# Kernel tuning notes

Measured on AMD Instinct MI355X. Metric: run time of the kernel, lower is better.

## Reference

```python
import jax, jax.numpy as jnp
import numpy as np

BN_EPS = 1e-5

def setup_inputs() -> dict:
    key = jax.random.key(0)
    ks = jax.random.split(key, 6)
    B, C, N = 8, 256, 4096
    da = C // 4
    return {
        "x": jax.random.normal(ks[0], (B, C, N), dtype=jnp.float32),
        "Wq": jax.random.normal(ks[1], (da, C), dtype=jnp.float32) * (C ** -0.5),
        "Wk": jax.random.normal(ks[2], (da, C), dtype=jnp.float32) * (C ** -0.5),
        "Wv": jax.random.normal(ks[3], (C, C), dtype=jnp.float32) * (C ** -0.5),
        "Wp": jax.random.normal(ks[4], (C, C), dtype=jnp.float32) * (C ** -0.5),
        "bn_gamma": jnp.ones((C,), dtype=jnp.float32),
        "bn_beta": jnp.zeros((C,), dtype=jnp.float32),
        "bn_mean": jnp.zeros((C,), dtype=jnp.float32),
        "bn_var": jnp.ones((C,), dtype=jnp.float32),
    }

def reference(x, Wq, Wk, Wv, Wp, bn_gamma, bn_beta, bn_mean, bn_var):
    # x: [B, C, N]; 1x1 Conv1d == channel matmul
    q = jnp.einsum('bcn,dc->bnd', x, Wq)          # [B, N, da]
    k = jnp.einsum('bcn,dc->bdn', x, Wk)          # [B, da, N]
    v = jnp.einsum('bcn,dc->bnd', x, Wv)          # [B, N, C]
    energy = jnp.einsum('bnd,bdm->bnm', q, k)     # [B, N, N]
    # offset-attention double normalization: softmax over dim=1 (rows), then L1 over dim=-1
    attn = jax.nn.softmax(energy, axis=1)
    attn = attn / (1e-9 + attn.sum(axis=-1, keepdims=True))
    fsa = jnp.einsum('bnm,bmc->bcn', attn, v)     # [B, C, N]
    y = x - fsa
    h = jnp.einsum('bcn,dc->bdn', y, Wp)          # 1x1 conv of LBR
    # BatchNorm1d (inference-mode with running stats)
    inv = bn_gamma / jnp.sqrt(bn_var + BN_EPS)
    h = h * inv[None, :, None] + (bn_beta - bn_mean * inv)[None, :, None]
    return jax.nn.relu(h) + x
```

## Files before the change

### kernel.cpp

```cpp
#include <hip/hip_runtime.h>
#include <math.h>

#define BD 8
#define CD 256
#define ND 4096
#define DA 64
#define CT 272

typedef __attribute__((ext_vector_type(8))) short short8v;
typedef __attribute__((ext_vector_type(4))) float float4v;

static __device__ __forceinline__ float4v mfma16(short8v a, short8v b, float4v c) {
  return __builtin_amdgcn_mfma_f32_16x16x32_bf16(a, b, c, 0, 0, 0);
}
static __device__ __forceinline__ unsigned short f2bf(float f) {
  union { float f; unsigned int u; } v; v.f = f;
  return (unsigned short)((v.u + 0x7fffu + ((v.u >> 16) & 1u)) >> 16);
}
static __device__ __forceinline__ float bf2f(unsigned short h) {
  union { unsigned int u; float f; } v; v.u = (unsigned int)h << 16;
  return v.f;
}
static __device__ __forceinline__ int sw(int row, int c8) {
  return row * 64 + (((c8) ^ (row & 7)) << 3);
}
typedef const __attribute__((address_space(1))) unsigned int g_u32;
typedef __attribute__((address_space(3))) unsigned int l_u32;
static __device__ __forceinline__ void gld16(const void* g, void* l) {
  __builtin_amdgcn_global_load_lds((g_u32*)g, (l_u32*)l, 16, 0, 0);
}

__global__ __launch_bounds__(256) void k_prep(const float* __restrict__ x,
                                              unsigned short* __restrict__ xTh,
                                              unsigned short* __restrict__ xTl) {
  const int n0 = blockIdx.x * 64, c0 = blockIdx.y * 64, b = blockIdx.z;
  __shared__ float Xs[64][68];
  const int tid = threadIdx.x;
  const int r0 = tid >> 4, col4 = (tid & 15) * 4;
#pragma unroll
  for (int j = 0; j < 4; ++j) {
    int r = r0 + j * 16;
    *(float4*)&Xs[r][col4] =
        *(const float4*)&x[((size_t)(b * CD + c0 + r)) * ND + n0 + col4];
  }
  __syncthreads();
  const int n = tid >> 2, cg = (tid & 3) * 16;
  unsigned short h[16], l[16];
#pragma unroll
  for (int j = 0; j < 16; ++j) {
    float v = Xs[cg + j][n];
    h[j] = f2bf(v);
    l[j] = f2bf(v - bf2f(h[j]));
  }
  size_t o = ((size_t)b * ND + n0 + n) * CD + c0 + cg;
#pragma unroll
  for (int j = 0; j < 4; ++j) {
    *(ushort4*)&xTh[o + j * 4] = *(ushort4*)&h[j * 4];
    *(ushort4*)&xTl[o + j * 4] = *(ushort4*)&l[j * 4];
  }
}

__global__ void k_prepW(const float* __restrict__ Wq, const float* __restrict__ Wk,
                        const float* __restrict__ Wv, const float* __restrict__ Wp,
                        unsigned short* Wqh, unsigned short* Wql,
                        unsigned short* Wkh, unsigned short* Wkl,
                        unsigned short* Wvh, unsigned short* Wvl,
                        unsigned short* Wph, unsigned short* Wpl) {
  int i = blockIdx.x * 256 + threadIdx.x;
  int row = i >> 6, c4 = (i & 63) * 4;
  const float* src; unsigned short *dh, *dl; int r;
  if (row < 64)       { src = Wq; dh = Wqh; dl = Wql; r = row; }
  else if (row < 128) { src = Wk; dh = Wkh; dl = Wkl; r = row - 64; }
  else if (row < 384) { src = Wv; dh = Wvh; dl = Wvl; r = row - 128; }
  else                { src = Wp; dh = Wph; dl = Wpl; r = row - 384; }
  float4 f = *(const float4*)&src[(size_t)r * 256 + c4];
  ushort4 hh, ll;
  hh.x = f2bf(f.x); hh.y = f2bf(f.y); hh.z = f2bf(f.z); hh.w = f2bf(f.w);
  ll.x = f2bf(f.x - bf2f(hh.x)); ll.y = f2bf(f.y - bf2f(hh.y));
  ll.z = f2bf(f.z - bf2f(hh.z)); ll.w = f2bf(f.w - bf2f(hh.w));
  *(ushort4*)&dh[(size_t)r * 256 + c4] = hh;
  *(ushort4*)&dl[(size_t)r * 256 + c4] = ll;
}

__global__ __launch_bounds__(256, 4) void k_proj64(
    const unsigned short* __restrict__ xTh, const unsigned short* __restrict__ xTl,
    const unsigned short* __restrict__ Wh, const unsigned short* __restrict__ Wl,
    unsigned short* __restrict__ oh, unsigned short* __restrict__ ol) {
  const int n0 = blockIdx.x * 128, b = blockIdx.y;
  const int tid = threadIdx.x, w = tid >> 6, lane = tid & 63, lq = lane & 15,
            quad = lane >> 4;
  const int nh = w & 1, dh = w >> 1;
  float4v O[2][4];
#pragma unroll
  for (int dt = 0; dt < 2; ++dt)
#pragma unroll
    for (int nt = 0; nt < 4; ++nt) O[dt][nt] = (float4v){0.f, 0.f, 0.f, 0.f};
#pragma unroll 2
  for (int ks = 0; ks < 8; ++ks) {
    short8v awh[2], awl[2], bxh[4], bxl[4];
#pragma unroll
    for (int dt = 0; dt < 2; ++dt) {
      size_t a = (size_t)(dh * 32 + dt * 16 + lq) * CD + ks * 32 + quad * 8;
      awh[dt] = *(const short8v*)(Wh + a);
      awl[dt] = *(const short8v*)(Wl + a);
    }
#pragma unroll
    for (int nt = 0; nt < 4; ++nt) {
      size_t a = ((size_t)b * ND + n0 + nh * 64 + nt * 16 + lq) * CD + ks * 32 + quad * 8;
      bxh[nt] = *(const short8v*)(xTh + a);
      bxl[nt] = *(const short8v*)(xTl + a);
    }
#pragma unroll
    for (int dt = 0; dt < 2; ++dt)
#pragma unroll
      for (int nt = 0; nt < 4; ++nt) {
        O[dt][nt] = mfma16(awh[dt], bxh[nt], O[dt][nt]);
        O[dt][nt] = mfma16(awl[dt], bxh[nt], O[dt][nt]);
        O[dt][nt] = mfma16(awh[dt], bxl[nt], O[dt][nt]);
      }
  }
#pragma unroll
  for (int dt = 0; dt < 2; ++dt)
#pragma unroll
    for (int nt = 0; nt < 4; ++nt) {
      int d0v = dh * 32 + dt * 16 + quad * 4;
      int n = n0 + nh * 64 + nt * 16 + lq;
      ushort4 hh, ll;
      float v0 = O[dt][nt][0], v1 = O[dt][nt][1], v2 = O[dt][nt][2], v3 = O[dt][nt][3];
      hh.x = f2bf(v0); hh.y = f2bf(v1); hh.z = f2bf(v2); hh.w = f2bf(v3);
      ll.x = f2bf(v0 - bf2f(hh.x)); ll.y = f2bf(v1 - bf2f(hh.y));
      ll.z = f2bf(v2 - bf2f(hh.z)); ll.w = f2bf(v3 - bf2f(hh.w));
      size_t o = ((size_t)b * ND + n) * DA + d0v;
      *(ushort4*)&oh[o] = hh;
      *(ushort4*)&ol[o] = ll;
    }
}

__global__ __launch_bounds__(256, 4) void k_projvT(
    const unsigned short* __restrict__ xTh, const unsigned short* __restrict__ xTl,
    const unsigned short* __restrict__ Wvh, const unsigned short* __restrict__ Wvl,
    unsigned short* __restrict__ vT) {
  const int m0 = blockIdx.x * 128, cob = blockIdx.y * 64, b = blockIdx.z;
  const int tid = threadIdx.x, w = tid >> 6, lane = tid & 63, lq = lane & 15,
            quad = lane >> 4;
  const int mh = w & 1, ch2 = w >> 1;
  float4v O[2][4];
#pragma unroll
  for (int ct = 0; ct < 2; ++ct)
#pragma unroll
    for (int mt = 0; mt < 4; ++mt) O[ct][mt] = (float4v){0.f, 0.f, 0.f, 0.f};
#pragma unroll 2
  for (int ks = 0; ks < 8; ++ks) {
    short8v awh[2], awl[2], bxh[4], bxl[4];
#pragma unroll
    for (int ct = 0; ct < 2; ++ct) {
      size_t a = (size_t)(cob + ch2 * 32 + ct * 16 + lq) * CD + ks * 32 + quad * 8;
      awh[ct] = *(const short8v*)(Wvh + a);
      awl[ct] = *(const short8v*)(Wvl + a);
    }
#pragma unroll
    for (int mt = 0; mt < 4; ++mt) {
      size_t a = ((size_t)b * ND + m0 + mh * 64 + mt * 16 + lq) * CD + ks * 32 + quad * 8;
      bxh[mt] = *(const short8v*)(xTh + a);
      bxl[mt] = *(const short8v*)(xTl + a);
    }
#pragma unroll
    for (int ct = 0; ct < 2; ++ct)
#pragma unroll
      for (int mt = 0; mt < 4; ++mt) {
        O[ct][mt] = mfma16(awh[ct], bxh[mt], O[ct][mt]);
        O[ct][mt] = mfma16(awl[ct], bxh[mt], O[ct][mt]);
        O[ct][mt] = mfma16(awh[ct], bxl[mt], O[ct][mt]);
      }
  }
#pragma unroll
  for (int ct = 0; ct < 2; ++ct)
#pragma unroll
    for (int mt = 0; mt < 4; ++mt) {
      int m = m0 + mh * 64 + mt * 16 + lq;
#pragma unroll
      for (int r = 0; r < 4; ++r) {
        int co = cob + ch2 * 32 + ct * 16 + quad * 4 + r;
        vT[((size_t)b * CT + co) * ND + m] = f2bf(O[ct][mt][r]);
      }
    }
}

__global__ void k_fill(unsigned short* __restrict__ vT) {
  int i = blockIdx.x * 256 + threadIdx.x;
  int b = i >> 14, r = (i >> 10) & 15, n4 = i & 1023;
  unsigned short val = (r == 0) ? (unsigned short)0x3F80 : (unsigned short)0;
  ushort4 v; v.x = val; v.y = val; v.z = val; v.w = val;
  *(ushort4*)&vT[((size_t)b * CT + 256 + r) * ND + n4 * 4] = v;
}

__global__ __launch_bounds__(512, 4) void k_colsum(
    const unsigned short* __restrict__ qh, const unsigned short* __restrict__ ql,
    const unsigned short* __restrict__ kh, const unsigned short* __restrict__ kl,
    float* __restrict__ Dp) {
  const int bid = blockIdx.x, b = bid & 7, half = (bid >> 3) & 1,
            m0 = (bid >> 4) * 128;
  const int nbase = half * 2048;
  const int tid = threadIdx.x, w = tid >> 6, lane = tid & 63, lq = lane & 15,
            quad = lane >> 4;
  const int mq = w & 3, nh = w >> 2;
  __shared__ __align__(16) unsigned short qbuf[2][128 * 64];
  __shared__ float Cb[128];
  short8v bkh[2][2], bkl[2][2];
#pragma unroll
  for (int sub = 0; sub < 2; ++sub)
#pragma unroll
    for (int k = 0; k < 2; ++k) {
      size_t a = ((size_t)b * ND + m0 + mq * 32 + sub * 16 + lq) * DA + k * 32 + quad * 8;
      bkh[sub][k] = *(const short8v*)(kh + a);
      bkl[sub][k] = *(const short8v*)(kl + a);
    }
  uint4 sreg[2];
  const int srow = tid >> 3, sc8 = tid & 7;
  auto load_stage = [&](int nb) {
    sreg[0] = *(const uint4*)(qh + ((size_t)b * ND + nb + srow) * DA + sc8 * 8);
    sreg[1] = *(const uint4*)(ql + ((size_t)b * ND + nb + srow) * DA + sc8 * 8);
  };
  auto write_stage = [&](int buf) {
    *(uint4*)&qbuf[buf][sw(srow, sc8)] = sreg[0];
    *(uint4*)&qbuf[buf][sw(64 + srow, sc8)] = sreg[1];
  };
  load_stage(nbase); write_stage(0); load_stage(nbase + 64);
  __syncthreads();
  float cs0 = 0.f, cs1 = 0.f;
  for (int i = 0; i < 32; ++i) {
    const int cur = i & 1;
#pragma unroll
    for (int s = 0; s < 2; ++s) {
      short8v ah[2], al[2];
#pragma unroll
      for (int k = 0; k < 2; ++k) {
        ah[k] = *(const short8v*)&qbuf[cur][sw(nh * 32 + s * 16 + lq, k * 4 + quad)];
        al[k] = *(const short8v*)&qbuf[cur][sw(64 + nh * 32 + s * 16 + lq, k * 4 + quad)];
      }
#pragma unroll
      for (int sub = 0; sub < 2; ++sub) {
        float4v acc = {0.f, 0.f, 0.f, 0.f};
#pragma unroll
        for (int k = 0; k < 2; ++k) {
          acc = mfma16(ah[k], bkh[sub][k], acc);
          acc = mfma16(al[k], bkh[sub][k], acc);
          acc = mfma16(ah[k], bkl[sub][k], acc);
        }
        float e0 = __expf(acc[0]) + __expf(acc[1]) + __expf(acc[2]) + __expf(acc[3]);
        if (sub == 0) cs0 += e0; else cs1 += e0;
      }
    }
    if (i < 31) { write_stage(1 - cur); if (i < 30) load_stage(nbase + (i + 2) * 64); }
    __syncthreads();
  }
  cs0 += __shfl_down(cs0, 16); cs0 += __shfl_down(cs0, 32);
  cs1 += __shfl_down(cs1, 16); cs1 += __shfl_down(cs1, 32);
  if (nh == 0 && lane < 16) {
    Cb[mq * 32 + lane] = cs0;
    Cb[mq * 32 + 16 + lane] = cs1;
  }
  __syncthreads();
  if (nh == 1 && lane < 16) {
    float t0 = Cb[mq * 32 + lane] + cs0;
    float t1 = Cb[mq * 32 + 16 + lane] + cs1;
    size_t o = (size_t)half * (BD * ND) + (size_t)b * ND + m0 + mq * 32 + lane;
    Dp[o] = t0;
    Dp[o + 16] = t1;
  }
}

__global__ void k_rcp(const float* __restrict__ Dp, float* __restrict__ Drec) {
  int i = blockIdx.x * 256 + threadIdx.x;
  float4 a = *(const float4*)&Dp[(size_t)i * 4];
  float4 c = *(const float4*)&Dp[(size_t)(BD * ND) + (size_t)i * 4];
  float4 r;
  r.x = 1.f / (a.x + c.x); r.y = 1.f / (a.y + c.y);
  r.z = 1.f / (a.z + c.z); r.w = 1.f / (a.w + c.w);
  *(float4*)&Drec[(size_t)i * 4] = r;
}

__global__ __launch_bounds__(512, 2) void k_attn(
    const unsigned short* __restrict__ qh, const unsigned short* __restrict__ ql,
    const unsigned short* __restrict__ khp, const unsigned short* __restrict__ klp,
    const unsigned short* __restrict__ vT, const float* __restrict__ Drec,
    unsigned short* xhy, const unsigned short* __restrict__ xTl) {
  const int bid = blockIdx.x, b = bid & 7, n0 = (bid >> 3) * 128;
  const int tid = threadIdx.x, w = tid >> 6, lane = tid & 63, lq = lane & 15,
            quad = lane >> 4;
  const int nq = w & 3, ch = w >> 2;
  __shared__ __align__(16) unsigned short vbuf[3][CT * 64];
  __shared__ __align__(16) unsigned short Pb[2][128 * 64];
  __shared__ float DrecS[ND];
  __shared__ float Sb[128];

  short8v aq[2][2][2];
#pragma unroll
  for (int s = 0; s < 2; ++s)
#pragma unroll
    for (int k = 0; k < 2; ++k) {
      size_t a = ((size_t)b * ND + n0 + nq * 32 + s * 16 + lq) * DA + k * 32 + quad * 8;
      aq[s][k][0] = *(const short8v*)(qh + a);
      aq[s][k][1] = *(const short8v*)(ql + a);
    }
  float4v O[2][9];
#pragma unroll
  for (int s = 0; s < 2; ++s)
#pragma unroll
    for (int t = 0; t < 9; ++t) O[s][t] = (float4v){0.f, 0.f, 0.f, 0.f};

  auto stageV = [&](int mt, int vn) {
    unsigned short* base = &vbuf[vn][0];
#pragma unroll
    for (int j = 0; j < 4; ++j) {
      int cidx = tid + j * 512;
      int row = cidx >> 3, ckpos = cidx & 7;
      const unsigned short* src =
          vT + ((size_t)b * CT + row) * ND + mt * 64 + ((ckpos ^ (row & 7)) << 3);
      gld16(src, base + (size_t)(w * 64 + j * 512) * 8);
    }
    if (tid < 128) {
      int cidx = 2048 + tid;
      int row = cidx >> 3, ckpos = cidx & 7;
      const unsigned short* src =
          vT + ((size_t)b * CT + row) * ND + mt * 64 + ((ckpos ^ (row & 7)) << 3);
      gld16(src, base + (size_t)(2048 + w * 64) * 8);
    }
  };
  short8v kc[8], kn[8];
  auto kload = [&](short8v* dst, int mt) {
#pragma unroll
    for (int sub = 0; sub < 2; ++sub)
#pragma unroll
      for (int k = 0; k < 2; ++k) {
        size_t a = ((size_t)b * ND + mt * 64 + ch * 32 + sub * 16 + lq) * DA +
                   k * 32 + quad * 8;
        dst[sub * 4 + k * 2 + 0] = *(const short8v*)(khp + a);
        dst[sub * 4 + k * 2 + 1] = *(const short8v*)(klp + a);
      }
  };

  stageV(0, 0);
  kload(kc, 0);
  for (int idx = tid; idx < ND / 4; idx += 512)
    *(float4*)&DrecS[idx * 4] = *(const float4*)&Drec[(size_t)b * ND + idx * 4];
  __syncthreads();

  int vn = 0;
#pragma unroll 1
  for (int i = 0; i < 64; ++i) {
    int vnext = vn + 1; if (vnext == 3) vnext = 0;
    if (i < 63) { stageV(i + 1, vnext); kload(kn, i + 1); }
    unsigned short* Pcur = &Pb[i & 1][0];
#pragma unroll
    for (int sub = 0; sub < 2; ++sub) {
      const int m_loc = ch * 32 + sub * 16 + lq;
      const float dr = DrecS[(i << 6) + m_loc];
#pragma unroll
      for (int s = 0; s < 2; ++s) {
        float4v acc = {0.f, 0.f, 0.f, 0.f};
#pragma unroll
        for (int k = 0; k < 2; ++k) {
          acc = mfma16(aq[s][k][0], kc[sub * 4 + k * 2 + 0], acc);
          acc = mfma16(aq[s][k][1], kc[sub * 4 + k * 2 + 0], acc);
          acc = mfma16(aq[s][k][0], kc[sub * 4 + k * 2 + 1], acc);
        }
        const int nrow = nq * 32 + s * 16 + quad * 4;
#pragma unroll
        for (int r = 0; r < 4; ++r) {
          float p = __expf(acc[r]) * dr;
          const int n_loc = nrow + r;
          union { float f; unsigned int u; } pu; pu.f = p;
          Pcur[n_loc * 64 + ((((m_loc >> 3) ^ (n_loc & 7)) << 3) | (m_loc & 7))] =
              (unsigned short)(pu.u >> 16);
        }
      }
    }
    __syncthreads();
    const unsigned short* Pc = &Pb[i & 1][0];
    const unsigned short* vc = &vbuf[vn][0];
    short8v ap[2][2];
#pragma unroll
    for (int s = 0; s < 2; ++s)
#pragma unroll
      for (int k = 0; k < 2; ++k)
        ap[s][k] = *(const short8v*)&Pc[sw(nq * 32 + s * 16 + lq, k * 4 + quad)];
#pragma unroll
    for (int ti = 0; ti < 9; ++ti) {
      if (ch == 0 || ti < 8) {
        const int t = ch * 9 + ti;
#pragma unroll
        for (int k = 0; k < 2; ++k) {
          short8v bv = *(const short8v*)&vc[sw(t * 16 + lq, k * 4 + quad)];
#pragma unroll
          for (int s = 0; s < 2; ++s) O[s][ti] = mfma16(bv, ap[s][k], O[s][ti]);
        }
      }
    }
    if (i < 63) {
#pragma unroll
      for (int t = 0; t < 8; ++t) kc[t] = kn[t];
    }
    vn = vnext;
  }
  if (ch == 1 && quad == 0) {
#pragma unroll
    for (int s = 0; s < 2; ++s) Sb[nq * 32 + s * 16 + lq] = O[s][7][0];
  }
  __syncthreads();
  float rsc[2];
#pragma unroll
  for (int s = 0; s < 2; ++s)
    rsc[s] = 1.0f / (1e-9f + Sb[nq * 32 + s * 16 + lq]);
#pragma unroll
  for (int ti = 0; ti < 9; ++ti) {
    const bool active = (ch == 0) || (ti < 7);
    if (active) {
      const int t = ch * 9 + ti;
      const int cb = t * 16 + quad * 4;
#pragma unroll
      for (int s = 0; s < 2; ++s) {
        const int n = n0 + nq * 32 + s * 16 + lq;
        const size_t off = ((size_t)b * ND + n) * CD + cb;
        ushort4 h4 = *(const ushort4*)&xhy[off];
        ushort4 l4 = *(const ushort4*)&xTl[off];
        ushort4 o4;
        o4.x = f2bf(bf2f(h4.x) + bf2f(l4.x) - O[s][ti][0] * rsc[s]);
        o4.y = f2bf(bf2f(h4.y) + bf2f(l4.y) - O[s][ti][1] * rsc[s]);
        o4.z = f2bf(bf2f(h4.z) + bf2f(l4.z) - O[s][ti][2] * rsc[s]);
        o4.w = f2bf(bf2f(h4.w) + bf2f(l4.w) - O[s][ti][3] * rsc[s]);
        *(ushort4*)&xhy[off] = o4;
      }
    }
  }
}

__global__ __launch_bounds__(256) void k_final(const unsigned short* __restrict__ y,
                                               const unsigned short* __restrict__ Wpb,
                                               const float* __restrict__ x,
                                               const float* __restrict__ gamma,
                                               const float* __restrict__ beta,
                                               const float* __restrict__ mean,
                                               const float* __restrict__ var,
                                               float* __restrict__ out) {
  const int bid = blockIdx.x;
  const int b = bid & 7;
  const int rem = bid >> 3;
  const int n0 = (rem & 63) * 64;
  const int d0 = (rem >> 6) * 64;
  const int tid = threadIdx.x;
  const int wave = tid >> 6, lane = tid & 63, lq = lane & 15, quad = lane >> 4;
  const int dw = d0 + wave * 16;
  float4v O[4];
#pragma unroll
  for (int s = 0; s < 4; ++s) O[s] = (float4v){0.f, 0.f, 0.f, 0.f};
#pragma unroll
  for (int chh = 0; chh < 8; ++chh) {
    const size_t ab = (size_t)(dw + lq) * CD + chh * 32 + quad * 8;
    short8v a0 = *(const short8v*)(Wpb + ab);
#pragma unroll
    for (int s = 0; s < 4; ++s) {
      const size_t bb = ((size_t)b * ND + n0 + s * 16 + lq) * CD + chh * 32 + quad * 8;
      short8v bv = *(const short8v*)(y + bb);
      O[s] = mfma16(a0, bv, O[s]);
    }
  }
#pragma unroll
  for (int r = 0; r < 4; ++r) {
    const int d = dw + quad * 4 + r;
    const float inv  = gamma[d] / sqrtf(var[d] + 1e-5f);
    const float bias = beta[d] - mean[d] * inv;
#pragma unroll
    for (int s = 0; s < 4; ++s) {
      const int n = n0 + s * 16 + lq;
      const size_t oi = ((size_t)b * CD + d) * ND + n;
      out[oi] = fmaxf(O[s][r] * inv + bias, 0.f) + x[oi];
    }
  }
}

extern "C" void kernel_launch(void* const* d_in, const int* in_sizes, int n_in,
                              void* d_out, int out_size, void* d_ws, size_t ws_size,
                              hipStream_t stream) {
  const float* x     = (const float*)d_in[0];
  const float* Wq    = (const float*)d_in[1];
  const float* Wk    = (const float*)d_in[2];
  const float* Wv    = (const float*)d_in[3];
  const float* Wp    = (const float*)d_in[4];
  const float* gamma = (const float*)d_in[5];
  const float* beta  = (const float*)d_in[6];
  const float* mean  = (const float*)d_in[7];
  const float* var   = (const float*)d_in[8];
  float* out = (float*)d_out;

  char* wsp = (char*)d_ws;
  unsigned short* qh  = (unsigned short*)wsp; wsp += (size_t)BD * ND * DA * 2;
  unsigned short* ql  = (unsigned short*)wsp; wsp += (size_t)BD * ND * DA * 2;
  unsigned short* khp = (unsigned short*)wsp; wsp += (size_t)BD * ND * DA * 2;
  unsigned short* klp = (unsigned short*)wsp; wsp += (size_t)BD * ND * DA * 2;
  unsigned short* vT  = (unsigned short*)wsp; wsp += (size_t)BD * CT * ND * 2;
  unsigned short* xTh = (unsigned short*)wsp; wsp += (size_t)BD * ND * CD * 2;
  unsigned short* xTl = (unsigned short*)wsp; wsp += (size_t)BD * ND * CD * 2;
  unsigned short* Wqh = (unsigned short*)wsp; wsp += (size_t)64 * 256 * 2;
  unsigned short* Wql = (unsigned short*)wsp; wsp += (size_t)64 * 256 * 2;
  unsigned short* Wkh = (unsigned short*)wsp; wsp += (size_t)64 * 256 * 2;
  unsigned short* Wkl = (unsigned short*)wsp; wsp += (size_t)64 * 256 * 2;
  unsigned short* Wvh = (unsigned short*)wsp; wsp += (size_t)256 * 256 * 2;
  unsigned short* Wvl = (unsigned short*)wsp; wsp += (size_t)256 * 256 * 2;
  unsigned short* Wph = (unsigned short*)wsp; wsp += (size_t)256 * 256 * 2;
  unsigned short* Wpl = (unsigned short*)wsp; wsp += (size_t)256 * 256 * 2;
  float* Drec = (float*)wsp; wsp += (size_t)BD * ND * 4;
  float* Dp   = (float*)wsp; wsp += (size_t)2 * BD * ND * 4;
  unsigned short* y = xTh;

  dim3 blk(256), blk5(512);
  k_prep<<<dim3(ND / 64, CD / 64, BD), blk, 0, stream>>>(x, xTh, xTl);
  k_prepW<<<dim3(160), blk, 0, stream>>>(Wq, Wk, Wv, Wp, Wqh, Wql, Wkh, Wkl,
                                         Wvh, Wvl, Wph, Wpl);
  k_proj64<<<dim3(ND / 128, BD), blk, 0, stream>>>(xTh, xTl, Wqh, Wql, qh, ql);
  k_proj64<<<dim3(ND / 128, BD), blk, 0, stream>>>(xTh, xTl, Wkh, Wkl, khp, klp);
  k_projvT<<<dim3(ND / 128, 4, BD), blk, 0, stream>>>(xTh, xTl, Wvh, Wvl, vT);
  k_fill<<<dim3(512), blk, 0, stream>>>(vT);
  k_colsum<<<dim3(512), blk5, 0, stream>>>(qh, ql, khp, klp, Dp);
  k_rcp<<<dim3(32), blk, 0, stream>>>(Dp, Drec);
  k_attn<<<dim3(256), blk5, 0, stream>>>(qh, ql, khp, klp, vT, Drec, y, xTl);
  k_final<<<dim3(2048), blk, 0, stream>>>(y, Wph, x, gamma, beta, mean, var, out);
}
```

Measured before the change: 519.9 us.

## Fuse Q/K/V projections, drop q low part, restructure attention tiling

```diff
diff --git a/kernel.cpp b/kernel.cpp
--- a/kernel.cpp
+++ b/kernel.cpp
@@ -5,7 +5,6 @@
 #define CD 256
 #define ND 4096
 #define DA 64
-#define CT 272
 
 typedef __attribute__((ext_vector_type(8))) short short8v;
 typedef __attribute__((ext_vector_type(4))) float float4v;
@@ -62,149 +61,103 @@
 
 __global__ void k_prepW(const float* __restrict__ Wq, const float* __restrict__ Wk,
                         const float* __restrict__ Wv, const float* __restrict__ Wp,
-                        unsigned short* Wqh, unsigned short* Wql,
-                        unsigned short* Wkh, unsigned short* Wkl,
-                        unsigned short* Wvh, unsigned short* Wvl,
+                        unsigned short* Wch, unsigned short* Wcl,
                         unsigned short* Wph, unsigned short* Wpl) {
   int i = blockIdx.x * 256 + threadIdx.x;
   int row = i >> 6, c4 = (i & 63) * 4;
-  const float* src; unsigned short *dh, *dl; int r;
-  if (row < 64)       { src = Wq; dh = Wqh; dl = Wql; r = row; }
-  else if (row < 128) { src = Wk; dh = Wkh; dl = Wkl; r = row - 64; }
-  else if (row < 384) { src = Wv; dh = Wvh; dl = Wvl; r = row - 128; }
-  else                { src = Wp; dh = Wph; dl = Wpl; r = row - 384; }
+  const float* src; unsigned short *dh, *dl; int r, drow;
+  if (row < 64)       { src = Wq; r = row;       dh = Wch; dl = Wcl; drow = row; }
+  else if (row < 128) { src = Wk; r = row - 64;  dh = Wch; dl = Wcl; drow = row; }
+  else if (row < 384) { src = Wv; r = row - 128; dh = Wch; dl = Wcl; drow = row; }
+  else                { src = Wp; r = row - 384; dh = Wph; dl = Wpl; drow = row - 384; }
   float4 f = *(const float4*)&src[(size_t)r * 256 + c4];
   ushort4 hh, ll;
   hh.x = f2bf(f.x); hh.y = f2bf(f.y); hh.z = f2bf(f.z); hh.w = f2bf(f.w);
   ll.x = f2bf(f.x - bf2f(hh.x)); ll.y = f2bf(f.y - bf2f(hh.y));
   ll.z = f2bf(f.z - bf2f(hh.z)); ll.w = f2bf(f.w - bf2f(hh.w));
-  *(ushort4*)&dh[(size_t)r * 256 + c4] = hh;
-  *(ushort4*)&dl[(size_t)r * 256 + c4] = ll;
-}
-
-__global__ __launch_bounds__(256, 4) void k_proj64(
+  *(ushort4*)&dh[(size_t)drow * 256 + c4] = hh;
+  *(ushort4*)&dl[(size_t)drow * 256 + c4] = ll;
+}
+
+__global__ __launch_bounds__(512) void k_proj(
     const unsigned short* __restrict__ xTh, const unsigned short* __restrict__ xTl,
-    const unsigned short* __restrict__ Wh, const unsigned short* __restrict__ Wl,
-    unsigned short* __restrict__ oh, unsigned short* __restrict__ ol) {
+    const unsigned short* __restrict__ Wch, const unsigned short* __restrict__ Wcl,
+    unsigned short* __restrict__ qh, unsigned short* __restrict__ kh,
+    unsigned short* __restrict__ kl, unsigned short* __restrict__ vT) {
   const int n0 = blockIdx.x * 128, b = blockIdx.y;
   const int tid = threadIdx.x, w = tid >> 6, lane = tid & 63, lq = lane & 15,
             quad = lane >> 4;
-  const int nh = w & 1, dh = w >> 1;
-  float4v O[2][4];
-#pragma unroll
-  for (int dt = 0; dt < 2; ++dt)
-#pragma unroll
-    for (int nt = 0; nt < 4; ++nt) O[dt][nt] = (float4v){0.f, 0.f, 0.f, 0.f};
-#pragma unroll 2
+  __shared__ __align__(16) unsigned short xs[2][2][128][40];
+  float4v O[24];
+#pragma unroll
+  for (int t = 0; t < 24; ++t) O[t] = (float4v){0.f, 0.f, 0.f, 0.f};
+
+  const int srow = tid >> 2, sc4 = tid & 3;
+  uint4 rh, rl;
+  auto load_slice = [&](int ks) {
+    size_t a = ((size_t)b * ND + n0 + srow) * CD + ks * 32 + sc4 * 8;
+    rh = *(const uint4*)(xTh + a);
+    rl = *(const uint4*)(xTl + a);
+  };
+  auto write_slice = [&](int buf) {
+    *(uint4*)&xs[buf][0][srow][sc4 * 8] = rh;
+    *(uint4*)&xs[buf][1][srow][sc4 * 8] = rl;
+  };
+  load_slice(0); write_slice(0);
+#pragma unroll 1
   for (int ks = 0; ks < 8; ++ks) {
-    short8v awh[2], awl[2], bxh[4], bxl[4];
-#pragma unroll
-    for (int dt = 0; dt < 2; ++dt) {
-      size_t a = (size_t)(dh * 32 + dt * 16 + lq) * CD + ks * 32 + quad * 8;
-      awh[dt] = *(const short8v*)(Wh + a);
-      awl[dt] = *(const short8v*)(Wl + a);
-    }
-#pragma unroll
-    for (int nt = 0; nt < 4; ++nt) {
-      size_t a = ((size_t)b * ND + n0 + nh * 64 + nt * 16 + lq) * CD + ks * 32 + quad * 8;
-      bxh[nt] = *(const short8v*)(xTh + a);
-      bxl[nt] = *(const short8v*)(xTl + a);
-    }
-#pragma unroll
-    for (int dt = 0; dt < 2; ++dt)
-#pragma unroll
-      for (int nt = 0; nt < 4; ++nt) {
-        O[dt][nt] = mfma16(awh[dt], bxh[nt], O[dt][nt]);
-        O[dt][nt] = mfma16(awl[dt], bxh[nt], O[dt][nt]);
-        O[dt][nt] = mfma16(awh[dt], bxl[nt], O[dt][nt]);
-      }
-  }
-#pragma unroll
-  for (int dt = 0; dt < 2; ++dt)
-#pragma unroll
-    for (int nt = 0; nt < 4; ++nt) {
-      int d0v = dh * 32 + dt * 16 + quad * 4;
-      int n = n0 + nh * 64 + nt * 16 + lq;
+    __syncthreads();
+    if (ks < 7) load_slice(ks + 1);
+    short8v bxh = *(const short8v*)&xs[ks & 1][0][w * 16 + lq][quad * 8];
+    short8v bxl = *(const short8v*)&xs[ks & 1][1][w * 16 + lq][quad * 8];
+#pragma unroll
+    for (int t = 0; t < 24; ++t) {
+      size_t a = (size_t)(t * 16 + lq) * CD + ks * 32 + quad * 8;
+      short8v awh = *(const short8v*)(Wch + a);
+      short8v awl = *(const short8v*)(Wcl + a);
+      O[t] = mfma16(awh, bxh, O[t]);
+      O[t] = mfma16(awl, bxh, O[t]);
+      O[t] = mfma16(awh, bxl, O[t]);
+    }
+    if (ks < 7) write_slice((ks + 1) & 1);
+  }
+  const int n = n0 + w * 16 + lq;
+#pragma unroll
+  for (int t = 0; t < 24; ++t) {
+    if (t < 4) {
+      ushort4 hh;
+      hh.x = f2bf(O[t][0]); hh.y = f2bf(O[t][1]);
+      hh.z = f2bf(O[t][2]); hh.w = f2bf(O[t][3]);
+      *(ushort4*)&qh[((size_t)b * ND + n) * DA + t * 16 + quad * 4] = hh;
+    } else if (t < 8) {
       ushort4 hh, ll;
-      float v0 = O[dt][nt][0], v1 = O[dt][nt][1], v2 = O[dt][nt][2], v3 = O[dt][nt][3];
-      hh.x = f2bf(v0); hh.y = f2bf(v1); hh.z = f2bf(v2); hh.w = f2bf(v3);
-      ll.x = f2bf(v0 - bf2f(hh.x)); ll.y = f2bf(v1 - bf2f(hh.y));
-      ll.z = f2bf(v2 - bf2f(hh.z)); ll.w = f2bf(v3 - bf2f(hh.w));
-      size_t o = ((size_t)b * ND + n) * DA + d0v;
-      *(ushort4*)&oh[o] = hh;
-      *(ushort4*)&ol[o] = ll;
-    }
-}
-
-__global__ __launch_bounds__(256, 4) void k_projvT(
-    const unsigned short* __restrict__ xTh, const unsigned short* __restrict__ xTl,
-    const unsigned short* __restrict__ Wvh, const unsigned short* __restrict__ Wvl,
-    unsigned short* __restrict__ vT) {
-  const int m0 = blockIdx.x * 128, cob = blockIdx.y * 64, b = blockIdx.z;
-  const int tid = threadIdx.x, w = tid >> 6, lane = tid & 63, lq = lane & 15,
-            quad = lane >> 4;
-  const int mh = w & 1, ch2 = w >> 1;
-  float4v O[2][4];
-#pragma unroll
-  for (int ct = 0; ct < 2; ++ct)
-#pragma unroll
-    for (int mt = 0; mt < 4; ++mt) O[ct][mt] = (float4v){0.f, 0.f, 0.f, 0.f};
-#pragma unroll 2
-  for (int ks = 0; ks < 8; ++ks) {
-    short8v awh[2], awl[2], bxh[4], bxl[4];
-#pragma unroll
-    for (int ct = 0; ct < 2; ++ct) {
-      size_t a = (size_t)(cob + ch2 * 32 + ct * 16 + lq) * CD + ks * 32 + quad * 8;
-      awh[ct] = *(const short8v*)(Wvh + a);
-      awl[ct] = *(const short8v*)(Wvl + a);
-    }
-#pragma unroll
-    for (int mt = 0; mt < 4; ++mt) {
-      size_t a = ((size_t)b * ND + m0 + mh * 64 + mt * 16 + lq) * CD + ks * 32 + quad * 8;
-      bxh[mt] = *(const short8v*)(xTh + a);
-      bxl[mt] = *(const short8v*)(xTl + a);
-    }
-#pragma unroll
-    for (int ct = 0; ct < 2; ++ct)
-#pragma unroll
-      for (int mt = 0; mt < 4; ++mt) {
-        O[ct][mt] = mfma16(awh[ct], bxh[mt], O[ct][mt]);
-        O[ct][mt] = mfma16(awl[ct], bxh[mt], O[ct][mt]);
-        O[ct][mt] = mfma16(awh[ct], bxl[mt], O[ct][mt]);
-      }
-  }
-#pragma unroll
-  for (int ct = 0; ct < 2; ++ct)
-#pragma unroll
-    for (int mt = 0; mt < 4; ++mt) {
-      int m = m0 + mh * 64 + mt * 16 + lq;
+      hh.x = f2bf(O[t][0]); hh.y = f2bf(O[t][1]);
+      hh.z = f2bf(O[t][2]); hh.w = f2bf(O[t][3]);
+      ll.x = f2bf(O[t][0] - bf2f(hh.x)); ll.y = f2bf(O[t][1] - bf2f(hh.y));
+      ll.z = f2bf(O[t][2] - bf2f(hh.z)); ll.w = f2bf(O[t][3] - bf2f(hh.w));
+      size_t o = ((size_t)b * ND + n) * DA + (t - 4) * 16 + quad * 4;
+      *(ushort4*)&kh[o] = hh;
+      *(ushort4*)&kl[o] = ll;
+    } else {
 #pragma unroll
       for (int r = 0; r < 4; ++r) {
-        int co = cob + ch2 * 32 + ct * 16 + quad * 4 + r;
-        vT[((size_t)b * CT + co) * ND + m] = f2bf(O[ct][mt][r]);
-      }
-    }
-}
-
-__global__ void k_fill(unsigned short* __restrict__ vT) {
-  int i = blockIdx.x * 256 + threadIdx.x;
-  int b = i >> 14, r = (i >> 10) & 15, n4 = i & 1023;
-  unsigned short val = (r == 0) ? (unsigned short)0x3F80 : (unsigned short)0;
-  ushort4 v; v.x = val; v.y = val; v.z = val; v.w = val;
-  *(ushort4*)&vT[((size_t)b * CT + 256 + r) * ND + n4 * 4] = v;
+        int c = (t - 8) * 16 + quad * 4 + r;
+        vT[((size_t)b * CD + c) * ND + n] = f2bf(O[t][r]);
+      }
+    }
+  }
 }
 
 __global__ __launch_bounds__(512, 4) void k_colsum(
-    const unsigned short* __restrict__ qh, const unsigned short* __restrict__ ql,
-    const unsigned short* __restrict__ kh, const unsigned short* __restrict__ kl,
-    float* __restrict__ Dp) {
+    const unsigned short* __restrict__ qh, const unsigned short* __restrict__ khp,
+    const unsigned short* __restrict__ klp, float* __restrict__ Dp) {
   const int bid = blockIdx.x, b = bid & 7, half = (bid >> 3) & 1,
             m0 = (bid >> 4) * 128;
   const int nbase = half * 2048;
   const int tid = threadIdx.x, w = tid >> 6, lane = tid & 63, lq = lane & 15,
             quad = lane >> 4;
   const int mq = w & 3, nh = w >> 2;
-  __shared__ __align__(16) unsigned short qbuf[2][128 * 64];
+  __shared__ __align__(16) unsigned short qbuf[2][64 * 64];
   __shared__ float Cb[128];
   short8v bkh[2][2], bkl[2][2];
 #pragma unroll
@@ -212,39 +165,35 @@
 #pragma unroll
     for (int k = 0; k < 2; ++k) {
       size_t a = ((size_t)b * ND + m0 + mq * 32 + sub * 16 + lq) * DA + k * 32 + quad * 8;
-      bkh[sub][k] = *(const short8v*)(kh + a);
-      bkl[sub][k] = *(const short8v*)(kl + a);
-    }
-  uint4 sreg[2];
+      bkh[sub][k] = *(const short8v*)(khp + a);
+      bkl[sub][k] = *(const short8v*)(klp + a);
+    }
+  uint4 sreg;
   const int srow = tid >> 3, sc8 = tid & 7;
   auto load_stage = [&](int nb) {
-    sreg[0] = *(const uint4*)(qh + ((size_t)b * ND + nb + srow) * DA + sc8 * 8);
-    sreg[1] = *(const uint4*)(ql + ((size_t)b * ND + nb + srow) * DA + sc8 * 8);
+    sreg = *(const uint4*)(qh + ((size_t)b * ND + nb + srow) * DA + sc8 * 8);
   };
   auto write_stage = [&](int buf) {
-    *(uint4*)&qbuf[buf][sw(srow, sc8)] = sreg[0];
-    *(uint4*)&qbuf[buf][sw(64 + srow, sc8)] = sreg[1];
+    *(uint4*)&qbuf[buf][sw(srow, sc8)] = sreg;
   };
   load_stage(nbase); write_stage(0); load_stage(nbase + 64);
   __syncthreads();
   float cs0 = 0.f, cs1 = 0.f;
+#pragma unroll 1
   for (int i = 0; i < 32; ++i) {
     const int cur = i & 1;
 #pragma unroll
     for (int s = 0; s < 2; ++s) {
-      short8v ah[2], al[2];
-#pragma unroll
-      for (int k = 0; k < 2; ++k) {
+      short8v ah[2];
+#pragma unroll
+      for (int k = 0; k < 2; ++k)
         ah[k] = *(const short8v*)&qbuf[cur][sw(nh * 32 + s * 16 + lq, k * 4 + quad)];
-        al[k] = *(const short8v*)&qbuf[cur][sw(64 + nh * 32 + s * 16 + lq, k * 4 + quad)];
-      }
 #pragma unroll
       for (int sub = 0; sub < 2; ++sub) {
         float4v acc = {0.f, 0.f, 0.f, 0.f};
 #pragma unroll
         for (int k = 0; k < 2; ++k) {
           acc = mfma16(ah[k], bkh[sub][k], acc);
-          acc = mfma16(al[k], bkh[sub][k], acc);
           acc = mfma16(ah[k], bkl[sub][k], acc);
         }
         float e0 = __expf(acc[0]) + __expf(acc[1]) + __expf(acc[2]) + __expf(acc[3]);
@@ -280,158 +229,129 @@
   *(float4*)&Drec[(size_t)i * 4] = r;
 }
 
-__global__ __launch_bounds__(512, 2) void k_attn(
-    const unsigned short* __restrict__ qh, const unsigned short* __restrict__ ql,
-    const unsigned short* __restrict__ khp, const unsigned short* __restrict__ klp,
-    const unsigned short* __restrict__ vT, const float* __restrict__ Drec,
-    unsigned short* xhy, const unsigned short* __restrict__ xTl) {
-  const int bid = blockIdx.x, b = bid & 7, n0 = (bid >> 3) * 128;
+__global__ __launch_bounds__(512, 4) void k_attn(
+    const unsigned short* __restrict__ qh, const unsigned short* __restrict__ khp,
+    const unsigned short* __restrict__ klp, const unsigned short* __restrict__ vT,
+    const float* __restrict__ Drec, unsigned short* xhy,
+    const unsigned short* __restrict__ xTl) {
+  const int bid = blockIdx.x, b = bid & 7, n0 = (bid >> 3) * 64;
   const int tid = threadIdx.x, w = tid >> 6, lane = tid & 63, lq = lane & 15,
             quad = lane >> 4;
   const int nq = w & 3, ch = w >> 2;
-  __shared__ __align__(16) unsigned short vbuf[3][CT * 64];
-  __shared__ __align__(16) unsigned short Pb[2][128 * 64];
-  __shared__ float DrecS[ND];
-  __shared__ float Sb[128];
-
-  short8v aq[2][2][2];
-#pragma unroll
-  for (int s = 0; s < 2; ++s)
-#pragma unroll
-    for (int k = 0; k < 2; ++k) {
-      size_t a = ((size_t)b * ND + n0 + nq * 32 + s * 16 + lq) * DA + k * 32 + quad * 8;
-      aq[s][k][0] = *(const short8v*)(qh + a);
-      aq[s][k][1] = *(const short8v*)(ql + a);
-    }
-  float4v O[2][9];
-#pragma unroll
-  for (int s = 0; s < 2; ++s)
-#pragma unroll
-    for (int t = 0; t < 9; ++t) O[s][t] = (float4v){0.f, 0.f, 0.f, 0.f};
-
-  auto stageV = [&](int mt, int vn) {
-    unsigned short* base = &vbuf[vn][0];
+  __shared__ __align__(16) unsigned char arena[2 * 32768 + 8192];
+  unsigned short* vbuf0 = (unsigned short*)arena;
+  unsigned short* vbuf1 = (unsigned short*)(arena + 32768);
+  unsigned short* Pb    = (unsigned short*)(arena + 65536);
+  float* Sb             = (float*)(arena + 65536);
+
+  short8v aq[2];
+#pragma unroll
+  for (int k = 0; k < 2; ++k)
+    aq[k] = *(const short8v*)(qh + ((size_t)b * ND + n0 + nq * 16 + lq) * DA +
+                              k * 32 + quad * 8);
+  float4v O[8];
+#pragma unroll
+  for (int t = 0; t < 8; ++t) O[t] = (float4v){0.f, 0.f, 0.f, 0.f};
+  float rs[4] = {0.f, 0.f, 0.f, 0.f};
+
+  auto stageV = [&](int mt, unsigned short* base) {
 #pragma unroll
     for (int j = 0; j < 4; ++j) {
       int cidx = tid + j * 512;
       int row = cidx >> 3, ckpos = cidx & 7;
       const unsigned short* src =
-          vT + ((size_t)b * CT + row) * ND + mt * 64 + ((ckpos ^ (row & 7)) << 3);
+          vT + ((size_t)b * CD + row) * ND + mt * 64 + ((ckpos ^ (row & 7)) << 3);
       gld16(src, base + (size_t)(w * 64 + j * 512) * 8);
     }
-    if (tid < 128) {
-      int cidx = 2048 + tid;
-      int row = cidx >> 3, ckpos = cidx & 7;
-      const unsigned short* src =
-          vT + ((size_t)b * CT + row) * ND + mt * 64 + ((ckpos ^ (row & 7)) << 3);
-      gld16(src, base + (size_t)(2048 + w * 64) * 8);
-    }
   };
-  short8v kc[8], kn[8];
-  auto kload = [&](short8v* dst, int mt) {
-#pragma unroll
-    for (int sub = 0; sub < 2; ++sub)
-#pragma unroll
-      for (int k = 0; k < 2; ++k) {
-        size_t a = ((size_t)b * ND + mt * 64 + ch * 32 + sub * 16 + lq) * DA +
-                   k * 32 + quad * 8;
-        dst[sub * 4 + k * 2 + 0] = *(const short8v*)(khp + a);
-        dst[sub * 4 + k * 2 + 1] = *(const short8v*)(klp + a);
-      }
-  };
-
-  stageV(0, 0);
-  kload(kc, 0);
-  for (int idx = tid; idx < ND / 4; idx += 512)
-    *(float4*)&DrecS[idx * 4] = *(const float4*)&Drec[(size_t)b * ND + idx * 4];
-  __syncthreads();
-
-  int vn = 0;
+
+  stageV(0, vbuf0);
+  __syncthreads();
+
 #pragma unroll 1
   for (int i = 0; i < 64; ++i) {
-    int vnext = vn + 1; if (vnext == 3) vnext = 0;
-    if (i < 63) { stageV(i + 1, vnext); kload(kn, i + 1); }
-    unsigned short* Pcur = &Pb[i & 1][0];
+    const int mg0 = (i << 6) + ch * 32;
+    short8v kch[2][2], kcl[2][2];
+#pragma unroll
+    for (int sub = 0; sub < 2; ++sub)
+#pragma unroll
+      for (int k = 0; k < 2; ++k) {
+        size_t a = ((size_t)b * ND + mg0 + sub * 16 + lq) * DA + k * 32 + quad * 8;
+        kch[sub][k] = *(const short8v*)(khp + a);
+        kcl[sub][k] = *(const short8v*)(klp + a);
+      }
+    float dr[2];
+#pragma unroll
+    for (int sub = 0; sub < 2; ++sub)
+      dr[sub] = Drec[(size_t)b * ND + mg0 + sub * 16 + lq];
 #pragma unroll
     for (int sub = 0; sub < 2; ++sub) {
+      float4v acc = {0.f, 0.f, 0.f, 0.f};
+#pragma unroll
+      for (int k = 0; k < 2; ++k) {
+        acc = mfma16(aq[k], kch[sub][k], acc);
+        acc = mfma16(aq[k], kcl[sub][k], acc);
+      }
       const int m_loc = ch * 32 + sub * 16 + lq;
-      const float dr = DrecS[(i << 6) + m_loc];
-#pragma unroll
-      for (int s = 0; s < 2; ++s) {
-        float4v acc = {0.f, 0.f, 0.f, 0.f};
-#pragma unroll
-        for (int k = 0; k < 2; ++k) {
-          acc = mfma16(aq[s][k][0], kc[sub * 4 + k * 2 + 0], acc);
-          acc = mfma16(aq[s][k][1], kc[sub * 4 + k * 2 + 0], acc);
-          acc = mfma16(aq[s][k][0], kc[sub * 4 + k * 2 + 1], acc);
-        }
-        const int nrow = nq * 32 + s * 16 + quad * 4;
-#pragma unroll
-        for (int r = 0; r < 4; ++r) {
-          float p = __expf(acc[r]) * dr;
-          const int n_loc = nrow + r;
-          union { float f; unsigned int u; } pu; pu.f = p;
-          Pcur[n_loc * 64 + ((((m_loc >> 3) ^ (n_loc & 7)) << 3) | (m_loc & 7))] =
-              (unsigned short)(pu.u >> 16);
-        }
+#pragma unroll
+      for (int r = 0; r < 4; ++r) {
+        float p = __expf(acc[r]) * dr[sub];
+        rs[r] += p;
+        const int n_loc = nq * 16 + quad * 4 + r;
+        union { float f; unsigned int u; } pu; pu.f = p;
+        Pb[n_loc * 64 + ((((m_loc >> 3) ^ (n_loc & 7)) << 3) | (m_loc & 7))] =
+            (unsigned short)(pu.u >> 16);
       }
     }
     __syncthreads();
-    const unsigned short* Pc = &Pb[i & 1][0];
-    const unsigned short* vc = &vbuf[vn][0];
-    short8v ap[2][2];
-#pragma unroll
-    for (int s = 0; s < 2; ++s)
-#pragma unroll
-      for (int k = 0; k < 2; ++k)
-        ap[s][k] = *(const short8v*)&Pc[sw(nq * 32 + s * 16 + lq, k * 4 + quad)];
-#pragma unroll
-    for (int ti = 0; ti < 9; ++ti) {
-      if (ch == 0 || ti < 8) {
-        const int t = ch * 9 + ti;
-#pragma unroll
-        for (int k = 0; k < 2; ++k) {
-          short8v bv = *(const short8v*)&vc[sw(t * 16 + lq, k * 4 + quad)];
-#pragma unroll
-          for (int s = 0; s < 2; ++s) O[s][ti] = mfma16(bv, ap[s][k], O[s][ti]);
-        }
-      }
-    }
-    if (i < 63) {
-#pragma unroll
-      for (int t = 0; t < 8; ++t) kc[t] = kn[t];
-    }
-    vn = vnext;
-  }
-  if (ch == 1 && quad == 0) {
-#pragma unroll
-    for (int s = 0; s < 2; ++s) Sb[nq * 32 + s * 16 + lq] = O[s][7][0];
-  }
-  __syncthreads();
-  float rsc[2];
-#pragma unroll
-  for (int s = 0; s < 2; ++s)
-    rsc[s] = 1.0f / (1e-9f + Sb[nq * 32 + s * 16 + lq]);
-#pragma unroll
-  for (int ti = 0; ti < 9; ++ti) {
-    const bool active = (ch == 0) || (ti < 7);
-    if (active) {
-      const int t = ch * 9 + ti;
-      const int cb = t * 16 + quad * 4;
-#pragma unroll
-      for (int s = 0; s < 2; ++s) {
-        const int n = n0 + nq * 32 + s * 16 + lq;
-        const size_t off = ((size_t)b * ND + n) * CD + cb;
-        ushort4 h4 = *(const ushort4*)&xhy[off];
-        ushort4 l4 = *(const ushort4*)&xTl[off];
-        ushort4 o4;
-        o4.x = f2bf(bf2f(h4.x) + bf2f(l4.x) - O[s][ti][0] * rsc[s]);
-        o4.y = f2bf(bf2f(h4.y) + bf2f(l4.y) - O[s][ti][1] * rsc[s]);
-        o4.z = f2bf(bf2f(h4.z) + bf2f(l4.z) - O[s][ti][2] * rsc[s]);
-        o4.w = f2bf(bf2f(h4.w) + bf2f(l4.w) - O[s][ti][3] * rsc[s]);
-        *(ushort4*)&xhy[off] = o4;
-      }
-    }
+    unsigned short* vc = (i & 1) ? vbuf1 : vbuf0;
+    if (i < 63) stageV(i + 1, (i & 1) ? vbuf0 : vbuf1);
+    short8v ap[2];
+#pragma unroll
+    for (int k = 0; k < 2; ++k)
+      ap[k] = *(const short8v*)&Pb[sw(nq * 16 + lq, k * 4 + quad)];
+#pragma unroll
+    for (int t = 0; t < 8; ++t) {
+      const int trow = (ch * 8 + t) * 16 + lq;
+#pragma unroll
+      for (int k = 0; k < 2; ++k) {
+        short8v bv = *(const short8v*)&vc[sw(trow, k * 4 + quad)];
+        O[t] = mfma16(bv, ap[k], O[t]);
+      }
+    }
+    __syncthreads();
+  }
+#pragma unroll
+  for (int r = 0; r < 4; ++r) {
+    rs[r] += __shfl_xor(rs[r], 1);
+    rs[r] += __shfl_xor(rs[r], 2);
+    rs[r] += __shfl_xor(rs[r], 4);
+    rs[r] += __shfl_xor(rs[r], 8);
+  }
+  if (ch == 0 && lq == 0) {
+#pragma unroll
+    for (int r = 0; r < 4; ++r) Sb[nq * 16 + quad * 4 + r] = rs[r];
+  }
+  __syncthreads();
+  if (ch == 1 && lq == 0) {
+#pragma unroll
+    for (int r = 0; r < 4; ++r) Sb[nq * 16 + quad * 4 + r] += rs[r];
+  }
+  __syncthreads();
+  const float rsc = 1.0f / (1e-9f + Sb[nq * 16 + lq]);
+  const int n = n0 + nq * 16 + lq;
+#pragma unroll
+  for (int t = 0; t < 8; ++t) {
+    const int cb = (ch * 8 + t) * 16 + quad * 4;
+    const size_t off = ((size_t)b * ND + n) * CD + cb;
+    ushort4 h4 = *(const ushort4*)&xhy[off];
+    ushort4 l4 = *(const ushort4*)&xTl[off];
+    ushort4 o4;
+    o4.x = f2bf(bf2f(h4.x) + bf2f(l4.x) - O[t][0] * rsc);
+    o4.y = f2bf(bf2f(h4.y) + bf2f(l4.y) - O[t][1] * rsc);
+    o4.z = f2bf(bf2f(h4.z) + bf2f(l4.z) - O[t][2] * rsc);
+    o4.w = f2bf(bf2f(h4.w) + bf2f(l4.w) - O[t][3] * rsc);
+    *(ushort4*)&xhy[off] = o4;
   }
 }
 
@@ -494,19 +414,14 @@
   float* out = (float*)d_out;
 
   char* wsp = (char*)d_ws;
-  unsigned short* qh  = (unsigned short*)wsp; wsp += (size_t)BD * ND * DA * 2;
-  unsigned short* ql  = (unsigned short*)wsp; wsp += (size_t)BD * ND * DA * 2;
+  unsigned short* qhp = (unsigned short*)wsp; wsp += (size_t)BD * ND * DA * 2;
   unsigned short* khp = (unsigned short*)wsp; wsp += (size_t)BD * ND * DA * 2;
   unsigned short* klp = (unsigned short*)wsp; wsp += (size_t)BD * ND * DA * 2;
-  unsigned short* vT  = (unsigned short*)wsp; wsp += (size_t)BD * CT * ND * 2;
+  unsigned short* vT  = (unsigned short*)wsp; wsp += (size_t)BD * CD * ND * 2;
   unsigned short* xTh = (unsigned short*)wsp; wsp += (size_t)BD * ND * CD * 2;
   unsigned short* xTl = (unsigned short*)wsp; wsp += (size_t)BD * ND * CD * 2;
-  unsigned short* Wqh = (unsigned short*)wsp; wsp += (size_t)64 * 256 * 2;
-  unsigned short* Wql = (unsigned short*)wsp; wsp += (size_t)64 * 256 * 2;
-  unsigned short* Wkh = (unsigned short*)wsp; wsp += (size_t)64 * 256 * 2;
-  unsigned short* Wkl = (unsigned short*)wsp; wsp += (size_t)64 * 256 * 2;
-  unsigned short* Wvh = (unsigned short*)wsp; wsp += (size_t)256 * 256 * 2;
-  unsigned short* Wvl = (unsigned short*)wsp; wsp += (size_t)256 * 256 * 2;
+  unsigned short* Wch = (unsigned short*)wsp; wsp += (size_t)384 * 256 * 2;
+  unsigned short* Wcl = (unsigned short*)wsp; wsp += (size_t)384 * 256 * 2;
   unsigned short* Wph = (unsigned short*)wsp; wsp += (size_t)256 * 256 * 2;
   unsigned short* Wpl = (unsigned short*)wsp; wsp += (size_t)256 * 256 * 2;
   float* Drec = (float*)wsp; wsp += (size_t)BD * ND * 4;
@@ -515,14 +430,11 @@
 
   dim3 blk(256), blk5(512);
   k_prep<<<dim3(ND / 64, CD / 64, BD), blk, 0, stream>>>(x, xTh, xTl);
-  k_prepW<<<dim3(160), blk, 0, stream>>>(Wq, Wk, Wv, Wp, Wqh, Wql, Wkh, Wkl,
-                                         Wvh, Wvl, Wph, Wpl);
-  k_proj64<<<dim3(ND / 128, BD), blk, 0, stream>>>(xTh, xTl, Wqh, Wql, qh, ql);
-  k_proj64<<<dim3(ND / 128, BD), blk, 0, stream>>>(xTh, xTl, Wkh, Wkl, khp, klp);
-  k_projvT<<<dim3(ND / 128, 4, BD), blk, 0, stream>>>(xTh, xTl, Wvh, Wvl, vT);
-  k_fill<<<dim3(512), blk, 0, stream>>>(vT);
-  k_colsum<<<dim3(512), blk5, 0, stream>>>(qh, ql, khp, klp, Dp);
+  k_prepW<<<dim3(160), blk, 0, stream>>>(Wq, Wk, Wv, Wp, Wch, Wcl, Wph, Wpl);
+  k_proj<<<dim3(ND / 128, BD), blk5, 0, stream>>>(xTh, xTl, Wch, Wcl, qhp, khp,
+                                                  klp, vT);
+  k_colsum<<<dim3(512), blk5, 0, stream>>>(qhp, khp, klp, Dp);
   k_rcp<<<dim3(32), blk, 0, stream>>>(Dp, Drec);
-  k_attn<<<dim3(256), blk5, 0, stream>>>(qh, ql, khp, klp, vT, Drec, y, xTl);
+  k_attn<<<dim3(512), blk5, 0, stream>>>(qhp, khp, klp, vT, Drec, y, xTl);
   k_final<<<dim3(2048), blk, 0, stream>>>(y, Wph, x, gamma, beta, mean, var, out);
 }
```

New measurement: 581.5 us. 1.12x slower.
